# Kernel optimization log

Measured on AMD Instinct MI355X. Metric: run time of the kernel, lower is better.

Reference implementation:

```python
import jax, jax.numpy as jnp
import numpy as np

N_NODES = 50000


def gcn_conv(h, W, b, src, dst, n_nodes):
    # PyG GCNConv: h' = D^{-1/2} (A + I) D^{-1/2} (h @ W) + b
    h = h @ W  # [N, out]
    deg = jax.ops.segment_sum(jnp.ones_like(dst, dtype=h.dtype), dst, num_segments=n_nodes)
    dinv = jnp.where(deg > 0, jax.lax.rsqrt(deg), 0.0)  # [N]
    norm = dinv[src] * dinv[dst]  # [E]
    msg = h[src] * norm[:, None]  # [E, out]
    out = jax.ops.segment_sum(msg, dst, num_segments=n_nodes)
    return out + b


def setup_inputs() -> dict:
    key = jax.random.key(0)
    ks = jax.random.split(key, 12)
    N, E, P, D, H = N_NODES, 1600000, 200000, 128, 128
    s = lambda fan_in: 1.0 / np.sqrt(fan_in)
    return {
        "x": jax.random.normal(ks[0], (N, D), dtype=jnp.float32),
        "edge_index": jax.random.randint(ks[1], (2, E), 0, N, dtype=jnp.int32),
        "drug_pairs": jax.random.randint(ks[2], (P, 2), 0, N, dtype=jnp.int32),
        "W1": jax.random.normal(ks[3], (D, H), dtype=jnp.float32) * s(D),
        "b1": jnp.zeros((H,), dtype=jnp.float32),
        "W2": jax.random.normal(ks[4], (H, H), dtype=jnp.float32) * s(H),
        "b2": jnp.zeros((H,), dtype=jnp.float32),
        "Wh1": jax.random.normal(ks[5], (2 * H, H), dtype=jnp.float32) * s(2 * H),
        "bh1": jnp.zeros((H,), dtype=jnp.float32),
        "Wh2": jax.random.normal(ks[6], (H, 1), dtype=jnp.float32) * s(H),
        "bh2": jnp.zeros((1,), dtype=jnp.float32),
    }


def reference(x, edge_index, drug_pairs, W1, b1, W2, b2, Wh1, bh1, Wh2, bh2):
    n = x.shape[0]
    # add self-loops once (GCNConv default add_self_loops=True)
    loop = jnp.arange(n, dtype=edge_index.dtype)
    src = jnp.concatenate([edge_index[0], loop])
    dst = jnp.concatenate([edge_index[1], loop])

    h = jax.nn.relu(gcn_conv(x, W1, b1, src, dst, n))  # dropout = identity (eval)
    h = jax.nn.relu(gcn_conv(h, W2, b2, src, dst, n))

    combined = jnp.concatenate([h[drug_pairs[:, 0]], h[drug_pairs[:, 1]]], axis=1)  # [P, 2H]
    out = jax.nn.relu(combined @ Wh1 + bh1) @ Wh2 + bh2  # [P, 1]
    return out
```

## Files before the change

kernel.cpp:

```cpp
#include <hip/hip_runtime.h>
#include <hip/hip_fp16.h>


#define BSH 9
#define BSZ (1 << BSH)
#define MSB 4096
#define XPAD 132
#define HB 256

typedef __attribute__((ext_vector_type(8))) short bf16x8;
typedef __attribute__((ext_vector_type(4))) float f32x4;

__device__ __forceinline__ void acc8(uint4 u, float4& lo, float4& hi) {
  float2 f0 = __half22float2(((const __half2*)&u)[0]);
  float2 f1 = __half22float2(((const __half2*)&u)[1]);
  float2 f2 = __half22float2(((const __half2*)&u)[2]);
  float2 f3 = __half22float2(((const __half2*)&u)[3]);
  lo.x += f0.x; lo.y += f0.y; lo.z += f1.x; lo.w += f1.y;
  hi.x += f2.x; hi.y += f2.y; hi.z += f3.x; hi.w += f3.y;
}

__device__ __forceinline__ float4 h4_to_f4(uint2 u) {
  float2 fa = __half22float2(*(__half2*)&u.x);
  float2 fb = __half22float2(*(__half2*)&u.y);
  return make_float4(fa.x, fa.y, fb.x, fb.y);
}

__device__ __forceinline__ void split8(const float* v, bf16x8& hi, bf16x8& lo) {
#pragma unroll
  for (int j = 0; j < 8; ++j) {
    unsigned u = __float_as_uint(v[j]);
    hi[j] = (short)(u >> 16);
    float lf = v[j] - __uint_as_float(u & 0xffff0000u);
    lo[j] = (short)(__float_as_uint(lf) >> 16);
  }
}

__global__ __launch_bounds__(256) void k_prep_w(
    const float* __restrict__ W1, const float* __restrict__ W2,
    const float* __restrict__ Wh1, short* __restrict__ fragH,
    short* __restrict__ fragL, int* __restrict__ gcnt, int* __restrict__ gcur,
    int kb) {
  if (blockIdx.x == 32) {
    int t = threadIdx.x;
    if (t < kb) { gcnt[t] = 0; gcur[t] = 0; }
    return;
  }
  int g = blockIdx.x * 256 + threadIdx.x;
  int w = g >> 11;
  int rem = g & 2047;
  int lane = rem & 63;
  int ts = rem >> 6;
  int t = ts >> 2, s = ts & 3;
  int n = (t << 4) + (lane & 15);
  int k0 = s * 32 + (lane >> 4) * 8;
  const float* W = (w == 0) ? W1 : (w == 1) ? W2 : (w == 2) ? Wh1 : (Wh1 + 128 * 128);
  short h[8], l[8];
#pragma unroll
  for (int j = 0; j < 8; ++j) {
    float x = W[(k0 + j) * 128 + n];
    unsigned u = __float_as_uint(x);
    h[j] = (short)(u >> 16);
    float lf = x - __uint_as_float(u & 0xffff0000u);
    l[j] = (short)(__float_as_uint(lf) >> 16);
  }
  ((int4*)fragH)[g] = *(int4*)h;
  ((int4*)fragL)[g] = *(int4*)l;
}

__global__ __launch_bounds__(256) void k_hist(const int* __restrict__ dst,
                                              int* __restrict__ gcnt,
                                              int e, int kb) {
  __shared__ int h4[512];
  int tid = threadIdx.x, wid = tid >> 6;
  for (int t = tid; t < 512; t += 256) h4[t] = 0;
  __syncthreads();
  for (int i = blockIdx.x * 256 + tid; i < e; i += HB * 256) {
    int d = __builtin_nontemporal_load(&dst[i]);
    atomicAdd(&h4[wid * 128 + (d >> BSH)], 1);
  }
  __syncthreads();
  if (tid < kb)
    atomicAdd(&gcnt[tid], h4[tid] + h4[128 + tid] + h4[256 + tid] + h4[384 + tid]);
}

__device__ __forceinline__ void gemm_body(
    const float* __restrict__ X, const short* __restrict__ fragH,
    const short* __restrict__ fragL, const float* __restrict__ rowscale,
    __half* __restrict__ C16, int n, int bid, float* sX) {
  int tid = threadIdx.x;
  int row0 = bid * 64;
  const float2* X2 = (const float2*)(X + (size_t)row0 * 128);
#pragma unroll
  for (int it = 0; it < 16; ++it) {
    int t = it * 256 + tid;
    int r = t >> 6, c2 = t & 63;
    int gr = row0 + r;
    float2 v = (gr < n) ? X2[t] : make_float2(0.f, 0.f);
    *(float2*)&sX[r * XPAD + c2 * 2] = v;
  }
  __syncthreads();
  int wid = tid >> 6, lane = tid & 63;
  int r0 = row0 + wid * 16;
  if (r0 >= n) return;
  int m = lane & 15, quad = lane >> 4;
  const float* xrow = sX + (wid * 16 + m) * XPAD;
  f32x4 acc[8];
#pragma unroll
  for (int t = 0; t < 8; ++t) acc[t] = (f32x4)(0.f);
  const int4* FH = (const int4*)fragH;
  const int4* FL = (const int4*)fragL;
#pragma unroll
  for (int s = 0; s < 4; ++s) {
    int k0 = s * 32 + quad * 8;
    float xv[8];
    *(float2*)&xv[0] = *(const float2*)(xrow + k0);
    *(float2*)&xv[2] = *(const float2*)(xrow + k0 + 2);
    *(float2*)&xv[4] = *(const float2*)(xrow + k0 + 4);
    *(float2*)&xv[6] = *(const float2*)(xrow + k0 + 6);
    bf16x8 ah, al;
    split8(xv, ah, al);
#pragma unroll
    for (int t = 0; t < 8; ++t) {
      int idx = (t * 4 + s) * 64 + lane;
      bf16x8 bh = *(const bf16x8*)&FH[idx];
      bf16x8 bl = *(const bf16x8*)&FL[idx];
      acc[t] = __builtin_amdgcn_mfma_f32_16x16x32_bf16(ah, bh, acc[t], 0, 0, 0);
      acc[t] = __builtin_amdgcn_mfma_f32_16x16x32_bf16(al, bh, acc[t], 0, 0, 0);
      acc[t] = __builtin_amdgcn_mfma_f32_16x16x32_bf16(ah, bl, acc[t], 0, 0, 0);
    }
  }
  float sc[4];
#pragma unroll
  for (int r = 0; r < 4; ++r)
    sc[r] = rowscale ? rowscale[r0 + quad * 4 + r] : 1.f;
#pragma unroll
  for (int t = 0; t < 8; ++t) {
#pragma unroll
    for (int r = 0; r < 4; ++r) {
      int row = r0 + quad * 4 + r;
      C16[(size_t)row * 128 + t * 16 + m] = __float2half(acc[t][r] * sc[r]);
    }
  }
}

__global__ __launch_bounds__(256) void k_gemm_mfma(
    const float* __restrict__ X, const short* __restrict__ fragH,
    const short* __restrict__ fragL, const float* __restrict__ rowscale,
    __half* __restrict__ C16, int n) {
  __shared__ float sX[64 * XPAD];
  gemm_body(X, fragH, fragL, rowscale, C16, n, blockIdx.x, sX);
}

__global__ __launch_bounds__(256) void k_multisplit(const int* __restrict__ src,
                                                    const int* __restrict__ dst,
                                                    const int* __restrict__ gcnt,
                                                    int* __restrict__ gcur,
                                                    int* __restrict__ tmp,
                                                    int e, int kb) {
  __shared__ int h4[4 * 128], off[4 * 128], sbase[128], ws[2];
  int tid = threadIdx.x, wid = tid >> 6, lane = tid & 63;
  for (int t = tid; t < 512; t += 256) h4[t] = 0;
  __syncthreads();
  int i0 = blockIdx.x * MSB + tid;
  int d[16], rk[16];
#pragma unroll
  for (int u = 0; u < 16; ++u) {
    int i = i0 + u * 256;
    if (i < e) {
      d[u] = __builtin_nontemporal_load(&dst[i]);
      rk[u] = atomicAdd(&h4[wid * 128 + (d[u] >> BSH)], 1);
    }
  }
  __syncthreads();
  int tot = 0;
  if (tid < 128) {
    int c0 = h4[tid], c1 = h4[128 + tid], c2 = h4[256 + tid], c3 = h4[384 + tid];
    off[tid] = 0; off[128 + tid] = c0;
    off[256 + tid] = c0 + c1; off[384 + tid] = c0 + c1 + c2;
    tot = c0 + c1 + c2 + c3;
  }
  int v = (tid < 128 && tid < kb) ? gcnt[tid] : 0;
  int orig = v;
#pragma unroll
  for (int o = 1; o < 64; o <<= 1) {
    int u = __shfl_up(v, o, 64);
    if (lane >= o) v += u;
  }
  if (lane == 63 && wid < 2) ws[wid] = v;
  __syncthreads();
  if (tid < 128) sbase[tid] = ((wid == 1) ? ws[0] : 0) + v - orig;
  __syncthreads();
  if (tid < kb && tot > 0) sbase[tid] += atomicAdd(&gcur[tid], tot);
  __syncthreads();
#pragma unroll
  for (int u = 0; u < 16; ++u) {
    int i = i0 + u * 256;
    if (i < e) {
      int s = __builtin_nontemporal_load(&src[i]);
      int k = d[u] >> BSH;
      tmp[sbase[k] + off[wid * 128 + k] + rk[u]] = ((d[u] & (BSZ - 1)) << 16) | s;
    }
  }
}

__global__ __launch_bounds__(512) void k_bucket_build(
    const int* __restrict__ tmp, const int* __restrict__ gcnt,
    int* __restrict__ rowptr, float* __restrict__ dinv,
    unsigned short* __restrict__ colarr, int n, int kb, int e) {
  __shared__ int dl[BSZ], cl[BSZ], sbase[128], ws[8];
  int t = threadIdx.x, b = blockIdx.x;
  int lane = t & 63, w = t >> 6;
  int v = (t < 128 && t < kb) ? gcnt[t] : 0;
  int orig0 = v;
#pragma unroll
  for (int o = 1; o < 64; o <<= 1) {
    int u = __shfl_up(v, o, 64);
    if (lane >= o) v += u;
  }
  if (lane == 63 && w < 2) ws[w] = v;
  dl[t] = 0;
  __syncthreads();
  if (t < 128) sbase[t] = ((w == 1) ? ws[0] : 0) + v - orig0;
  __syncthreads();
  int s0 = sbase[b];
  int s1 = s0 + gcnt[b];
  for (int j = s0 + t; j < s1; j += 512)
    atomicAdd(&dl[((unsigned)tmp[j]) >> 16], 1);
  __syncthreads();
  int dv = dl[t], orig = dv;
#pragma unroll
  for (int o = 1; o < 64; o <<= 1) {
    int u = __shfl_up(dv, o, 64);
    if (lane >= o) dv += u;
  }
  if (lane == 63) ws[w] = dv;
  __syncthreads();
  if (t == 0) {
    int a = 0;
#pragma unroll
    for (int k = 0; k < 8; ++k) { int x = ws[k]; ws[k] = a; a += x; }
  }
  __syncthreads();
  int ex = ws[w] + dv - orig;
  cl[t] = ex;
  int node = (b << BSH) + t;
  if (node < n) {
    rowptr[node] = s0 + ex;
    dinv[node] = rsqrtf((float)(orig + 1));
  }
  if (b == kb - 1 && t == 0) rowptr[n] = e;
  __syncthreads();
  for (int j = s0 + t; j < s1; j += 512) {
    int p = tmp[j];
    int r = atomicAdd(&cl[((unsigned)p) >> 16], 1);
    colarr[s0 + r] = (unsigned short)(p & 0xFFFF);
  }
}

__global__ __launch_bounds__(256) void k_gemm_dual(
    const float* __restrict__ X,
    const short* __restrict__ fHa, const short* __restrict__ fLa,
    const short* __restrict__ fHb, const short* __restrict__ fLb,
    __half* __restrict__ A16, __half* __restrict__ B16, int n) {
  __shared__ float sX[64 * XPAD];
  int tid = threadIdx.x;
  int row0 = blockIdx.x * 64;
  const float2* X2 = (const float2*)(X + (size_t)row0 * 128);
#pragma unroll
  for (int it = 0; it < 16; ++it) {
    int t = it * 256 + tid;
    int r = t >> 6, c2 = t & 63;
    int gr = row0 + r;
    float2 v = (gr < n) ? X2[t] : make_float2(0.f, 0.f);
    *(float2*)&sX[r * XPAD + c2 * 2] = v;
  }
  __syncthreads();
  int wid = tid >> 6, lane = tid & 63;
  int r0 = row0 + wid * 16;
  if (r0 >= n) return;
  int m = lane & 15, quad = lane >> 4;
  const float* xrow = sX + (wid * 16 + m) * XPAD;
  f32x4 accA[8], accB[8];
#pragma unroll
  for (int t = 0; t < 8; ++t) { accA[t] = (f32x4)(0.f); accB[t] = (f32x4)(0.f); }
  const int4* FHa = (const int4*)fHa; const int4* FLa = (const int4*)fLa;
  const int4* FHb = (const int4*)fHb; const int4* FLb = (const int4*)fLb;
#pragma unroll
  for (int s = 0; s < 4; ++s) {
    int k0 = s * 32 + quad * 8;
    float xv[8];
    *(float2*)&xv[0] = *(const float2*)(xrow + k0);
    *(float2*)&xv[2] = *(const float2*)(xrow + k0 + 2);
    *(float2*)&xv[4] = *(const float2*)(xrow + k0 + 4);
    *(float2*)&xv[6] = *(const float2*)(xrow + k0 + 6);
    bf16x8 ah, al;
    split8(xv, ah, al);
#pragma unroll
    for (int t = 0; t < 8; ++t) {
      int idx = (t * 4 + s) * 64 + lane;
      bf16x8 bha = *(const bf16x8*)&FHa[idx];
      bf16x8 bla = *(const bf16x8*)&FLa[idx];
      accA[t] = __builtin_amdgcn_mfma_f32_16x16x32_bf16(ah, bha, accA[t], 0, 0, 0);
      accA[t] = __builtin_amdgcn_mfma_f32_16x16x32_bf16(al, bha, accA[t], 0, 0, 0);
      accA[t] = __builtin_amdgcn_mfma_f32_16x16x32_bf16(ah, bla, accA[t], 0, 0, 0);
      bf16x8 bhb = *(const bf16x8*)&FHb[idx];
      bf16x8 blb = *(const bf16x8*)&FLb[idx];
      accB[t] = __builtin_amdgcn_mfma_f32_16x16x32_bf16(ah, bhb, accB[t], 0, 0, 0);
      accB[t] = __builtin_amdgcn_mfma_f32_16x16x32_bf16(al, bhb, accB[t], 0, 0, 0);
      accB[t] = __builtin_amdgcn_mfma_f32_16x16x32_bf16(ah, blb, accB[t], 0, 0, 0);
    }
  }
#pragma unroll
  for (int t = 0; t < 8; ++t) {
#pragma unroll
    for (int r = 0; r < 4; ++r) {
      int row = r0 + quad * 4 + r;
      A16[(size_t)row * 128 + t * 16 + m] = __float2half(accA[t][r]);
      B16[(size_t)row * 128 + t * 16 + m] = __float2half(accB[t][r]);
    }
  }
}

__global__ __launch_bounds__(256) void k_agg_h(
    const __half2* __restrict__ g2, const float* __restrict__ dinv,
    const int* __restrict__ rowptr, const unsigned short* __restrict__ col,
    const float* __restrict__ bias, float* __restrict__ out, int n) {
  int i = blockIdx.x * 4 + (threadIdx.x >> 6);
  if (i >= n) return;
  int lane = threadIdx.x & 63;
  int sub = lane >> 4;
  int c8 = lane & 15;
  const uint4* G = (const uint4*)g2;
  float4 z = make_float4(0.f, 0.f, 0.f, 0.f);
  float4 lo0 = z, lo1 = z, lo2 = z, lo3 = z, hi0 = z, hi1 = z, hi2 = z, hi3 = z;
  if (sub == 0) acc8(G[(size_t)i * 16 + c8], lo0, hi0);
  int beg = rowptr[i], end = rowptr[i + 1];
  int j = beg;
  for (; j + 16 <= end; j += 16) {
    int s0 = __builtin_nontemporal_load(&col[j + sub]);
    int s1 = __builtin_nontemporal_load(&col[j + 4 + sub]);
    int s2 = __builtin_nontemporal_load(&col[j + 8 + sub]);
    int s3 = __builtin_nontemporal_load(&col[j + 12 + sub]);
    uint4 u0 = G[(size_t)s0 * 16 + c8];
    uint4 u1 = G[(size_t)s1 * 16 + c8];
    uint4 u2 = G[(size_t)s2 * 16 + c8];
    uint4 u3 = G[(size_t)s3 * 16 + c8];
    acc8(u0, lo0, hi0); acc8(u1, lo1, hi1);
    acc8(u2, lo2, hi2); acc8(u3, lo3, hi3);
  }
  for (; j + 4 <= end; j += 4) {
    int s0 = __builtin_nontemporal_load(&col[j + sub]);
    acc8(G[(size_t)s0 * 16 + c8], lo1, hi1);
  }
  int rem = end - j;
  if (sub < rem) {
    int s0 = __builtin_nontemporal_load(&col[j + sub]);
    acc8(G[(size_t)s0 * 16 + c8], lo2, hi2);
  }
  float4 lo, hi;
  lo.x = (lo0.x + lo1.x) + (lo2.x + lo3.x);
  lo.y = (lo0.y + lo1.y) + (lo2.y + lo3.y);
  lo.z = (lo0.z + lo1.z) + (lo2.z + lo3.z);
  lo.w = (lo0.w + lo1.w) + (lo2.w + lo3.w);
  hi.x = (hi0.x + hi1.x) + (hi2.x + hi3.x);
  hi.y = (hi0.y + hi1.y) + (hi2.y + hi3.y);
  hi.z = (hi0.z + hi1.z) + (hi2.z + hi3.z);
  hi.w = (hi0.w + hi1.w) + (hi2.w + hi3.w);
  lo.x += __shfl_down(lo.x, 32, 64); lo.x += __shfl_down(lo.x, 16, 64);
  lo.y += __shfl_down(lo.y, 32, 64); lo.y += __shfl_down(lo.y, 16, 64);
  lo.z += __shfl_down(lo.z, 32, 64); lo.z += __shfl_down(lo.z, 16, 64);
  lo.w += __shfl_down(lo.w, 32, 64); lo.w += __shfl_down(lo.w, 16, 64);
  hi.x += __shfl_down(hi.x, 32, 64); hi.x += __shfl_down(hi.x, 16, 64);
  hi.y += __shfl_down(hi.y, 32, 64); hi.y += __shfl_down(hi.y, 16, 64);
  hi.z += __shfl_down(hi.z, 32, 64); hi.z += __shfl_down(hi.z, 16, 64);
  hi.w += __shfl_down(hi.w, 32, 64); hi.w += __shfl_down(hi.w, 16, 64);
  if (sub == 0) {
    float di = dinv[i];
    float4 b0 = ((const float4*)bias)[2 * c8];
    float4 b1 = ((const float4*)bias)[2 * c8 + 1];
    float4 o0, o1;
    o0.x = fmaxf(fmaf(di, lo.x, b0.x), 0.f);
    o0.y = fmaxf(fmaf(di, lo.y, b0.y), 0.f);
    o0.z = fmaxf(fmaf(di, lo.z, b0.z), 0.f);
    o0.w = fmaxf(fmaf(di, lo.w, b0.w), 0.f);
    o1.x = fmaxf(fmaf(di, hi.x, b1.x), 0.f);
    o1.y = fmaxf(fmaf(di, hi.y, b1.y), 0.f);
    o1.z = fmaxf(fmaf(di, hi.z, b1.z), 0.f);
    o1.w = fmaxf(fmaf(di, hi.w, b1.w), 0.f);
    ((float4*)out)[(size_t)i * 32 + 2 * c8] = o0;
    ((float4*)out)[(size_t)i * 32 + 2 * c8 + 1] = o1;
  }
}

__global__ __launch_bounds__(256) void k_pairs_h(
    const __half2* __restrict__ A, const __half2* __restrict__ B,
    const int* __restrict__ pairs, const float* __restrict__ bh1,
    const float* __restrict__ wh2, const float* __restrict__ bh2,
    float* __restrict__ out, int P) {
  int p = blockIdx.x * 4 + (threadIdx.x >> 6);
  int lane = threadIdx.x & 63;
  if (p >= P) return;
  int sub = lane >> 5, c4 = lane & 31;
  int p0 = pairs[2 * p], p1 = pairs[2 * p + 1];
  const uint2* T4 = sub ? (const uint2*)B : (const uint2*)A;
  int row = sub ? p1 : p0;
  float4 v = h4_to_f4(T4[(size_t)row * 32 + c4]);
  v.x += __shfl_xor(v.x, 32, 64);
  v.y += __shfl_xor(v.y, 32, 64);
  v.z += __shfl_xor(v.z, 32, 64);
  v.w += __shfl_xor(v.w, 32, 64);
  float4 bi = ((const float4*)bh1)[c4];
  float4 wv = ((const float4*)wh2)[c4];
  float s = fmaxf(v.x + bi.x, 0.f) * wv.x + fmaxf(v.y + bi.y, 0.f) * wv.y +
            fmaxf(v.z + bi.z, 0.f) * wv.z + fmaxf(v.w + bi.w, 0.f) * wv.w;
#pragma unroll
  for (int o = 16; o > 0; o >>= 1) s += __shfl_down(s, o, 64);
  if (lane == 0) out[p] = s + bh2[0];
}

extern "C" void kernel_launch(void* const* d_in, const int* in_sizes, int n_in,
                              void* d_out, int out_size, void* d_ws, size_t ws_size,
                              hipStream_t stream) {
  const float* x   = (const float*)d_in[0];
  const int* ei    = (const int*)d_in[1];
  const int* pairs = (const int*)d_in[2];
  const float* W1  = (const float*)d_in[3];
  const float* b1  = (const float*)d_in[4];
  const float* W2  = (const float*)d_in[5];
  const float* b2  = (const float*)d_in[6];
  const float* Wh1 = (const float*)d_in[7];
  const float* bh1 = (const float*)d_in[8];
  const float* Wh2 = (const float*)d_in[9];
  const float* bh2 = (const float*)d_in[10];
  (void)n_in; (void)out_size; (void)ws_size;

  int N = in_sizes[0] / 128;
  int E = in_sizes[1] / 2;
  int P = in_sizes[2] / 2;
  const int* src = ei;
  const int* dst = ei + E;
  int KB = (N + BSZ - 1) >> BSH;

  char* wsp = (char*)d_ws;
  size_t off = 0;
  auto alloc = [&](size_t bytes) -> void* {
    void* p = wsp + off;
    off += (bytes + 255) & ~(size_t)255;
    return p;
  };
  __half* g16 = (__half*)alloc((size_t)N * 128 * 2);
  float* h1   = (float*)alloc((size_t)N * 128 * 4);
  float* h2   = (float*)alloc((size_t)N * 128 * 4);
  float* dinv = (float*)alloc((size_t)N * 4);
  int* rowptr = (int*)alloc((size_t)(N + 1) * 4);
  unsigned short* colarr = (unsigned short*)alloc((size_t)E * 2);
  int* tmp    = (int*)alloc((size_t)E * 4);
  short* fragH = (short*)alloc(4 * 2048 * 8 * 2);
  short* fragL = (short*)alloc(4 * 2048 * 8 * 2);
  int* gcnt  = (int*)alloc((size_t)(KB + 1) * 4);
  int* gcur  = (int*)alloc((size_t)(KB + 1) * 4);
  __half* A16 = g16;
  __half* B16 = (__half*)h1;
  short* fH_W1 = fragH + 0 * 16384;  short* fL_W1 = fragL + 0 * 16384;
  short* fH_W2 = fragH + 1 * 16384;  short* fL_W2 = fragL + 1 * 16384;
  short* fH_Wa = fragH + 2 * 16384;  short* fL_Wa = fragL + 2 * 16384;
  short* fH_Wb = fragH + 3 * 16384;  short* fL_Wb = fragL + 3 * 16384;

  int GB = (N + 63) / 64;
  int AB = (N + 3) / 4;

  k_prep_w<<<33, 256, 0, stream>>>(W1, W2, Wh1, fragH, fragL, gcnt, gcur, KB);
  k_hist<<<HB, 256, 0, stream>>>(dst, gcnt, E, KB);
  k_multisplit<<<(E + MSB - 1) / MSB, 256, 0, stream>>>(src, dst, gcnt, gcur,
                                                        tmp, E, KB);
  k_bucket_build<<<KB, 512, 0, stream>>>(tmp, gcnt, rowptr, dinv, colarr, N, KB, E);
  k_gemm_mfma<<<GB, 256, 0, stream>>>(x, fH_W1, fL_W1, dinv, g16, N);
  k_agg_h<<<AB, 256, 0, stream>>>((const __half2*)g16, dinv, rowptr, colarr, b1, h1, N);
  k_gemm_mfma<<<GB, 256, 0, stream>>>(h1, fH_W2, fL_W2, dinv, g16, N);
  k_agg_h<<<AB, 256, 0, stream>>>((const __half2*)g16, dinv, rowptr, colarr, b2, h2, N);
  k_gemm_dual<<<GB, 256, 0, stream>>>(h2, fH_Wa, fL_Wa, fH_Wb, fL_Wb, A16, B16, N);
  k_pairs_h<<<(P + 3) / 4, 256, 0, stream>>>((const __half2*)A16, (const __half2*)B16,
                                             pairs, bh1, Wh2, bh2, (float*)d_out, P);
}
```

Before: 377.2 us.

## Store hidden activations in fp16, use f16 MFMA, fuse first GEMM with histogram

Hidden activations h1/h2 are now written as fp16 instead of fp32. The second-layer and head GEMMs read them directly with f16 MFMA, using two MFMAs (hi/lo weight split) instead of three bf16 MFMAs and no LDS staging. The first GEMM no longer depends on dinv, so it runs in the same launch as the degree histogram and is placed before the CSR build. To compensate, the first aggregation applies the source-side dinv scale per edge with an extra gather. This halves activation traffic and removes MFMA work and a launch. In exchange it adds fp16 rounding of activations and extra scattered reads of dinv during aggregation.

```diff
diff --git a/kernel.cpp b/kernel.cpp
--- a/kernel.cpp
+++ b/kernel.cpp
@@ -9,15 +9,18 @@
 #define HB 256
 
 typedef __attribute__((ext_vector_type(8))) short bf16x8;
+typedef __attribute__((ext_vector_type(8))) _Float16 f16x8;
 typedef __attribute__((ext_vector_type(4))) float f32x4;
 
-__device__ __forceinline__ void acc8(uint4 u, float4& lo, float4& hi) {
+__device__ __forceinline__ void acc8s(uint4 u, float f, float4& lo, float4& hi) {
   float2 f0 = __half22float2(((const __half2*)&u)[0]);
   float2 f1 = __half22float2(((const __half2*)&u)[1]);
   float2 f2 = __half22float2(((const __half2*)&u)[2]);
   float2 f3 = __half22float2(((const __half2*)&u)[3]);
-  lo.x += f0.x; lo.y += f0.y; lo.z += f1.x; lo.w += f1.y;
-  hi.x += f2.x; hi.y += f2.y; hi.z += f3.x; hi.w += f3.y;
+  lo.x = fmaf(f, f0.x, lo.x); lo.y = fmaf(f, f0.y, lo.y);
+  lo.z = fmaf(f, f1.x, lo.z); lo.w = fmaf(f, f1.y, lo.w);
+  hi.x = fmaf(f, f2.x, hi.x); hi.y = fmaf(f, f2.y, hi.y);
+  hi.z = fmaf(f, f3.x, hi.z); hi.w = fmaf(f, f3.y, hi.w);
 }
 
 __device__ __forceinline__ float4 h4_to_f4(uint2 u) {
@@ -59,35 +62,25 @@
 #pragma unroll
   for (int j = 0; j < 8; ++j) {
     float x = W[(k0 + j) * 128 + n];
-    unsigned u = __float_as_uint(x);
-    h[j] = (short)(u >> 16);
-    float lf = x - __uint_as_float(u & 0xffff0000u);
-    l[j] = (short)(__float_as_uint(lf) >> 16);
+    if (w == 0) {
+      unsigned u = __float_as_uint(x);
+      h[j] = (short)(u >> 16);
+      float lf = x - __uint_as_float(u & 0xffff0000u);
+      l[j] = (short)(__float_as_uint(lf) >> 16);
+    } else {
+      __half hh = __float2half(x);
+      h[j] = __half_as_short(hh);
+      l[j] = __half_as_short(__float2half(x - __half2float(hh)));
+    }
   }
   ((int4*)fragH)[g] = *(int4*)h;
   ((int4*)fragL)[g] = *(int4*)l;
 }
 
-__global__ __launch_bounds__(256) void k_hist(const int* __restrict__ dst,
-                                              int* __restrict__ gcnt,
-                                              int e, int kb) {
-  __shared__ int h4[512];
-  int tid = threadIdx.x, wid = tid >> 6;
-  for (int t = tid; t < 512; t += 256) h4[t] = 0;
-  __syncthreads();
-  for (int i = blockIdx.x * 256 + tid; i < e; i += HB * 256) {
-    int d = __builtin_nontemporal_load(&dst[i]);
-    atomicAdd(&h4[wid * 128 + (d >> BSH)], 1);
-  }
-  __syncthreads();
-  if (tid < kb)
-    atomicAdd(&gcnt[tid], h4[tid] + h4[128 + tid] + h4[256 + tid] + h4[384 + tid]);
-}
-
-__device__ __forceinline__ void gemm_body(
+__device__ __forceinline__ void gemm1_body(
     const float* __restrict__ X, const short* __restrict__ fragH,
-    const short* __restrict__ fragL, const float* __restrict__ rowscale,
-    __half* __restrict__ C16, int n, int bid, float* sX) {
+    const short* __restrict__ fragL, __half* __restrict__ C16, int n,
+    int bid, float* sX) {
   int tid = threadIdx.x;
   int row0 = bid * 64;
   const float2* X2 = (const float2*)(X + (size_t)row0 * 128);
@@ -130,6 +123,67 @@
       acc[t] = __builtin_amdgcn_mfma_f32_16x16x32_bf16(ah, bl, acc[t], 0, 0, 0);
     }
   }
+#pragma unroll
+  for (int t = 0; t < 8; ++t) {
+#pragma unroll
+    for (int r = 0; r < 4; ++r) {
+      int row = r0 + quad * 4 + r;
+      C16[(size_t)row * 128 + t * 16 + m] = __float2half(acc[t][r]);
+    }
+  }
+}
+
+__global__ __launch_bounds__(256) void k_gemm_hist(
+    const float* __restrict__ X, const short* __restrict__ fragH,
+    const short* __restrict__ fragL, __half* __restrict__ C16, int n, int gb,
+    const int* __restrict__ dst, int* __restrict__ gcnt, int e, int kb) {
+  __shared__ float sX[64 * XPAD];
+  if ((int)blockIdx.x < gb) {
+    gemm1_body(X, fragH, fragL, C16, n, blockIdx.x, sX);
+    return;
+  }
+  int bid = blockIdx.x - gb;
+  int* h4 = (int*)sX;
+  int tid = threadIdx.x, wid = tid >> 6;
+  for (int t = tid; t < 512; t += 256) h4[t] = 0;
+  __syncthreads();
+  for (int i = bid * 256 + tid; i < e; i += HB * 256) {
+    int d = __builtin_nontemporal_load(&dst[i]);
+    atomicAdd(&h4[wid * 128 + (d >> BSH)], 1);
+  }
+  __syncthreads();
+  if (tid < kb)
+    atomicAdd(&gcnt[tid], h4[tid] + h4[128 + tid] + h4[256 + tid] + h4[384 + tid]);
+}
+
+__global__ __launch_bounds__(256) void k_gemm_f16(
+    const __half* __restrict__ X16, const short* __restrict__ fragH,
+    const short* __restrict__ fragL, const float* __restrict__ rowscale,
+    __half* __restrict__ C16, int n) {
+  int wid = threadIdx.x >> 6, lane = threadIdx.x & 63;
+  int r0 = (blockIdx.x * 4 + wid) * 16;
+  if (r0 >= n) return;
+  int m = lane & 15, quad = lane >> 4;
+  const uint4* Xr = (const uint4*)(X16 + (size_t)(r0 + m) * 128);
+  f32x4 acc[8];
+#pragma unroll
+  for (int t = 0; t < 8; ++t) acc[t] = (f32x4)(0.f);
+  const int4* FH = (const int4*)fragH;
+  const int4* FL = (const int4*)fragL;
+#pragma unroll
+  for (int s = 0; s < 4; ++s) {
+    uint4 av = Xr[quad + 4 * s];
+    f16x8 a = *(const f16x8*)&av;
+#pragma unroll
+    for (int t = 0; t < 8; ++t) {
+      int idx = (t * 4 + s) * 64 + lane;
+      int4 bhv = FH[idx], blv = FL[idx];
+      f16x8 bh = *(const f16x8*)&bhv;
+      f16x8 bl = *(const f16x8*)&blv;
+      acc[t] = __builtin_amdgcn_mfma_f32_16x16x32_f16(a, bh, acc[t], 0, 0, 0);
+      acc[t] = __builtin_amdgcn_mfma_f32_16x16x32_f16(a, bl, acc[t], 0, 0, 0);
+    }
+  }
   float sc[4];
 #pragma unroll
   for (int r = 0; r < 4; ++r)
@@ -144,12 +198,44 @@
   }
 }
 
-__global__ __launch_bounds__(256) void k_gemm_mfma(
-    const float* __restrict__ X, const short* __restrict__ fragH,
-    const short* __restrict__ fragL, const float* __restrict__ rowscale,
-    __half* __restrict__ C16, int n) {
-  __shared__ float sX[64 * XPAD];
-  gemm_body(X, fragH, fragL, rowscale, C16, n, blockIdx.x, sX);
+__global__ __launch_bounds__(256) void k_gemm_dual_f16(
+    const __half* __restrict__ X16,
+    const short* __restrict__ fHa, const short* __restrict__ fLa,
+    const short* __restrict__ fHb, const short* __restrict__ fLb,
+    __half* __restrict__ A16, __half* __restrict__ B16, int n) {
+  int wid = threadIdx.x >> 6, lane = threadIdx.x & 63;
+  int r0 = (blockIdx.x * 4 + wid) * 16;
+  if (r0 >= n) return;
+  int m = lane & 15, quad = lane >> 4;
+  const uint4* Xr = (const uint4*)(X16 + (size_t)(r0 + m) * 128);
+  f32x4 accA[8], accB[8];
+#pragma unroll
+  for (int t = 0; t < 8; ++t) { accA[t] = (f32x4)(0.f); accB[t] = (f32x4)(0.f); }
+  const int4* FHa = (const int4*)fHa; const int4* FLa = (const int4*)fLa;
+  const int4* FHb = (const int4*)fHb; const int4* FLb = (const int4*)fLb;
+#pragma unroll
+  for (int s = 0; s < 4; ++s) {
+    uint4 av = Xr[quad + 4 * s];
+    f16x8 a = *(const f16x8*)&av;
+#pragma unroll
+    for (int t = 0; t < 8; ++t) {
+      int idx = (t * 4 + s) * 64 + lane;
+      int4 v0 = FHa[idx], v1 = FLa[idx], v2 = FHb[idx], v3 = FLb[idx];
+      accA[t] = __builtin_amdgcn_mfma_f32_16x16x32_f16(a, *(const f16x8*)&v0, accA[t], 0, 0, 0);
+      accA[t] = __builtin_amdgcn_mfma_f32_16x16x32_f16(a, *(const f16x8*)&v1, accA[t], 0, 0, 0);
+      accB[t] = __builtin_amdgcn_mfma_f32_16x16x32_f16(a, *(const f16x8*)&v2, accB[t], 0, 0, 0);
+      accB[t] = __builtin_amdgcn_mfma_f32_16x16x32_f16(a, *(const f16x8*)&v3, accB[t], 0, 0, 0);
+    }
+  }
+#pragma unroll
+  for (int t = 0; t < 8; ++t) {
+#pragma unroll
+    for (int r = 0; r < 4; ++r) {
+      int row = r0 + quad * 4 + r;
+      A16[(size_t)row * 128 + t * 16 + m] = __float2half(accA[t][r]);
+      B16[(size_t)row * 128 + t * 16 + m] = __float2half(accB[t][r]);
+    }
+  }
 }
 
 __global__ __launch_bounds__(256) void k_multisplit(const int* __restrict__ src,
@@ -258,83 +344,22 @@
   }
 }
 
-__global__ __launch_bounds__(256) void k_gemm_dual(
-    const float* __restrict__ X,
-    const short* __restrict__ fHa, const short* __restrict__ fLa,
-    const short* __restrict__ fHb, const short* __restrict__ fLb,
-    __half* __restrict__ A16, __half* __restrict__ B16, int n) {
-  __shared__ float sX[64 * XPAD];
-  int tid = threadIdx.x;
-  int row0 = blockIdx.x * 64;
-  const float2* X2 = (const float2*)(X + (size_t)row0 * 128);
-#pragma unroll
-  for (int it = 0; it < 16; ++it) {
-    int t = it * 256 + tid;
-    int r = t >> 6, c2 = t & 63;
-    int gr = row0 + r;
-    float2 v = (gr < n) ? X2[t] : make_float2(0.f, 0.f);
-    *(float2*)&sX[r * XPAD + c2 * 2] = v;
-  }
-  __syncthreads();
-  int wid = tid >> 6, lane = tid & 63;
-  int r0 = row0 + wid * 16;
-  if (r0 >= n) return;
-  int m = lane & 15, quad = lane >> 4;
-  const float* xrow = sX + (wid * 16 + m) * XPAD;
-  f32x4 accA[8], accB[8];
-#pragma unroll
-  for (int t = 0; t < 8; ++t) { accA[t] = (f32x4)(0.f); accB[t] = (f32x4)(0.f); }
-  const int4* FHa = (const int4*)fHa; const int4* FLa = (const int4*)fLa;
-  const int4* FHb = (const int4*)fHb; const int4* FLb = (const int4*)fLb;
-#pragma unroll
-  for (int s = 0; s < 4; ++s) {
-    int k0 = s * 32 + quad * 8;
-    float xv[8];
-    *(float2*)&xv[0] = *(const float2*)(xrow + k0);
-    *(float2*)&xv[2] = *(const float2*)(xrow + k0 + 2);
-    *(float2*)&xv[4] = *(const float2*)(xrow + k0 + 4);
-    *(float2*)&xv[6] = *(const float2*)(xrow + k0 + 6);
-    bf16x8 ah, al;
-    split8(xv, ah, al);
-#pragma unroll
-    for (int t = 0; t < 8; ++t) {
-      int idx = (t * 4 + s) * 64 + lane;
-      bf16x8 bha = *(const bf16x8*)&FHa[idx];
-      bf16x8 bla = *(const bf16x8*)&FLa[idx];
-      accA[t] = __builtin_amdgcn_mfma_f32_16x16x32_bf16(ah, bha, accA[t], 0, 0, 0);
-      accA[t] = __builtin_amdgcn_mfma_f32_16x16x32_bf16(al, bha, accA[t], 0, 0, 0);
-      accA[t] = __builtin_amdgcn_mfma_f32_16x16x32_bf16(ah, bla, accA[t], 0, 0, 0);
-      bf16x8 bhb = *(const bf16x8*)&FHb[idx];
-      bf16x8 blb = *(const bf16x8*)&FLb[idx];
-      accB[t] = __builtin_amdgcn_mfma_f32_16x16x32_bf16(ah, bhb, accB[t], 0, 0, 0);
-      accB[t] = __builtin_amdgcn_mfma_f32_16x16x32_bf16(al, bhb, accB[t], 0, 0, 0);
-      accB[t] = __builtin_amdgcn_mfma_f32_16x16x32_bf16(ah, blb, accB[t], 0, 0, 0);
-    }
-  }
-#pragma unroll
-  for (int t = 0; t < 8; ++t) {
-#pragma unroll
-    for (int r = 0; r < 4; ++r) {
-      int row = r0 + quad * 4 + r;
-      A16[(size_t)row * 128 + t * 16 + m] = __float2half(accA[t][r]);
-      B16[(size_t)row * 128 + t * 16 + m] = __float2half(accB[t][r]);
-    }
-  }
-}
-
 __global__ __launch_bounds__(256) void k_agg_h(
     const __half2* __restrict__ g2, const float* __restrict__ dinv,
+    const float* __restrict__ srcscale,
     const int* __restrict__ rowptr, const unsigned short* __restrict__ col,
-    const float* __restrict__ bias, float* __restrict__ out, int n) {
+    const float* __restrict__ bias, __half* __restrict__ out16, int n) {
   int i = blockIdx.x * 4 + (threadIdx.x >> 6);
   if (i >= n) return;
   int lane = threadIdx.x & 63;
   int sub = lane >> 4;
   int c8 = lane & 15;
   const uint4* G = (const uint4*)g2;
+  float di = dinv[i];
   float4 z = make_float4(0.f, 0.f, 0.f, 0.f);
   float4 lo0 = z, lo1 = z, lo2 = z, lo3 = z, hi0 = z, hi1 = z, hi2 = z, hi3 = z;
-  if (sub == 0) acc8(G[(size_t)i * 16 + c8], lo0, hi0);
+  if (sub == 0)
+    acc8s(G[(size_t)i * 16 + c8], srcscale ? di : 1.f, lo0, hi0);
   int beg = rowptr[i], end = rowptr[i + 1];
   int j = beg;
   for (; j + 16 <= end; j += 16) {
@@ -342,21 +367,27 @@
     int s1 = __builtin_nontemporal_load(&col[j + 4 + sub]);
     int s2 = __builtin_nontemporal_load(&col[j + 8 + sub]);
     int s3 = __builtin_nontemporal_load(&col[j + 12 + sub]);
+    float f0 = srcscale ? srcscale[s0] : 1.f;
+    float f1 = srcscale ? srcscale[s1] : 1.f;
+    float f2 = srcscale ? srcscale[s2] : 1.f;
+    float f3 = srcscale ? srcscale[s3] : 1.f;
     uint4 u0 = G[(size_t)s0 * 16 + c8];
     uint4 u1 = G[(size_t)s1 * 16 + c8];
     uint4 u2 = G[(size_t)s2 * 16 + c8];
     uint4 u3 = G[(size_t)s3 * 16 + c8];
-    acc8(u0, lo0, hi0); acc8(u1, lo1, hi1);
-    acc8(u2, lo2, hi2); acc8(u3, lo3, hi3);
+    acc8s(u0, f0, lo0, hi0); acc8s(u1, f1, lo1, hi1);
+    acc8s(u2, f2, lo2, hi2); acc8s(u3, f3, lo3, hi3);
   }
   for (; j + 4 <= end; j += 4) {
     int s0 = __builtin_nontemporal_load(&col[j + sub]);
-    acc8(G[(size_t)s0 * 16 + c8], lo1, hi1);
+    float f0 = srcscale ? srcscale[s0] : 1.f;
+    acc8s(G[(size_t)s0 * 16 + c8], f0, lo1, hi1);
   }
   int rem = end - j;
   if (sub < rem) {
     int s0 = __builtin_nontemporal_load(&col[j + sub]);
-    acc8(G[(size_t)s0 * 16 + c8], lo2, hi2);
+    float f0 = srcscale ? srcscale[s0] : 1.f;
+    acc8s(G[(size_t)s0 * 16 + c8], f0, lo2, hi2);
   }
   float4 lo, hi;
   lo.x = (lo0.x + lo1.x) + (lo2.x + lo3.x);
@@ -376,20 +407,20 @@
   hi.z += __shfl_down(hi.z, 32, 64); hi.z += __shfl_down(hi.z, 16, 64);
   hi.w += __shfl_down(hi.w, 32, 64); hi.w += __shfl_down(hi.w, 16, 64);
   if (sub == 0) {
-    float di = dinv[i];
     float4 b0 = ((const float4*)bias)[2 * c8];
     float4 b1 = ((const float4*)bias)[2 * c8 + 1];
-    float4 o0, o1;
-    o0.x = fmaxf(fmaf(di, lo.x, b0.x), 0.f);
-    o0.y = fmaxf(fmaf(di, lo.y, b0.y), 0.f);
-    o0.z = fmaxf(fmaf(di, lo.z, b0.z), 0.f);
-    o0.w = fmaxf(fmaf(di, lo.w, b0.w), 0.f);
-    o1.x = fmaxf(fmaf(di, hi.x, b1.x), 0.f);
-    o1.y = fmaxf(fmaf(di, hi.y, b1.y), 0.f);
-    o1.z = fmaxf(fmaf(di, hi.z, b1.z), 0.f);
-    o1.w = fmaxf(fmaf(di, hi.w, b1.w), 0.f);
-    ((float4*)out)[(size_t)i * 32 + 2 * c8] = o0;
-    ((float4*)out)[(size_t)i * 32 + 2 * c8 + 1] = o1;
+    __half2 q0 = __floats2half2_rn(fmaxf(fmaf(di, lo.x, b0.x), 0.f),
+                                   fmaxf(fmaf(di, lo.y, b0.y), 0.f));
+    __half2 q1 = __floats2half2_rn(fmaxf(fmaf(di, lo.z, b0.z), 0.f),
+                                   fmaxf(fmaf(di, lo.w, b0.w), 0.f));
+    __half2 q2 = __floats2half2_rn(fmaxf(fmaf(di, hi.x, b1.x), 0.f),
+                                   fmaxf(fmaf(di, hi.y, b1.y), 0.f));
+    __half2 q3 = __floats2half2_rn(fmaxf(fmaf(di, hi.z, b1.z), 0.f),
+                                   fmaxf(fmaf(di, hi.w, b1.w), 0.f));
+    uint4 o;
+    o.x = *(unsigned*)&q0; o.y = *(unsigned*)&q1;
+    o.z = *(unsigned*)&q2; o.w = *(unsigned*)&q3;
+    ((uint4*)out16)[(size_t)i * 16 + c8] = o;
   }
 }
 
@@ -450,8 +481,8 @@
     return p;
   };
   __half* g16 = (__half*)alloc((size_t)N * 128 * 2);
-  float* h1   = (float*)alloc((size_t)N * 128 * 4);
-  float* h2   = (float*)alloc((size_t)N * 128 * 4);
+  __half* h1  = (__half*)alloc((size_t)N * 128 * 2);
+  __half* h2  = (__half*)alloc((size_t)N * 128 * 2);
   float* dinv = (float*)alloc((size_t)N * 4);
   int* rowptr = (int*)alloc((size_t)(N + 1) * 4);
   unsigned short* colarr = (unsigned short*)alloc((size_t)E * 2);
@@ -461,25 +492,29 @@
   int* gcnt  = (int*)alloc((size_t)(KB + 1) * 4);
   int* gcur  = (int*)alloc((size_t)(KB + 1) * 4);
   __half* A16 = g16;
-  __half* B16 = (__half*)h1;
+  __half* B16 = h1;
   short* fH_W1 = fragH + 0 * 16384;  short* fL_W1 = fragL + 0 * 16384;
   short* fH_W2 = fragH + 1 * 16384;  short* fL_W2 = fragL + 1 * 16384;
   short* fH_Wa = fragH + 2 * 16384;  short* fL_Wa = fragL + 2 * 16384;
   short* fH_Wb = fragH + 3 * 16384;  short* fL_Wb = fragL + 3 * 16384;
 
   int GB = (N + 63) / 64;
+  int GF = (N / 16 + 3) / 4;
   int AB = (N + 3) / 4;
 
   k_prep_w<<<33, 256, 0, stream>>>(W1, W2, Wh1, fragH, fragL, gcnt, gcur, KB);
-  k_hist<<<HB, 256, 0, stream>>>(dst, gcnt, E, KB);
+  k_gemm_hist<<<GB + HB, 256, 0, stream>>>(x, fH_W1, fL_W1, g16, N, GB,
+                                           dst, gcnt, E, KB);
   k_multisplit<<<(E + MSB - 1) / MSB, 256, 0, stream>>>(src, dst, gcnt, gcur,
                                                         tmp, E, KB);
   k_bucket_build<<<KB, 512, 0, stream>>>(tmp, gcnt, rowptr, dinv, colarr, N, KB, E);
-  k_gemm_mfma<<<GB, 256, 0, stream>>>(x, fH_W1, fL_W1, dinv, g16, N);
-  k_agg_h<<<AB, 256, 0, stream>>>((const __half2*)g16, dinv, rowptr, colarr, b1, h1, N);
-  k_gemm_mfma<<<GB, 256, 0, stream>>>(h1, fH_W2, fL_W2, dinv, g16, N);
-  k_agg_h<<<AB, 256, 0, stream>>>((const __half2*)g16, dinv, rowptr, colarr, b2, h2, N);
-  k_gemm_dual<<<GB, 256, 0, stream>>>(h2, fH_Wa, fL_Wa, fH_Wb, fL_Wb, A16, B16, N);
+  k_agg_h<<<AB, 256, 0, stream>>>((const __half2*)g16, dinv, dinv, rowptr,
+                                  colarr, b1, h1, N);
+  k_gemm_f16<<<GF, 256, 0, stream>>>(h1, fH_W2, fL_W2, dinv, g16, N);
+  k_agg_h<<<AB, 256, 0, stream>>>((const __half2*)g16, dinv, nullptr, rowptr,
+                                  colarr, b2, h2, N);
+  k_gemm_dual_f16<<<GF, 256, 0, stream>>>(h2, fH_Wa, fL_Wa, fH_Wb, fL_Wb,
+                                          A16, B16, N);
   k_pairs_h<<<(P + 3) / 4, 256, 0, stream>>>((const __half2*)A16, (const __half2*)B16,
                                              pairs, bh1, Wh2, bh2, (float*)d_out, P);
 }
```

New measurement: 394.9 us. 1.05x slower.
